# Kernel optimization log

Measured on AMD Instinct MI355X. Metric: run time of the kernel, lower is better.

The kernel has to match this reference:

```python
import jax, jax.numpy as jnp
import numpy as np

B, T_TEXT, HID = 16, 512, 512
MAX_LEN = 2048
DP_CH, DP_K = 256, 3
PP_CH, PP_K, PP_LAYERS = 384, 5, 5
N_BINS = 256


def conv1d_same(x, w, b, pad):
    # x: [B, C_in, T], w: [C_out, C_in, K] -> [B, C_out, T]
    xp = jnp.pad(x, ((0, 0), (0, 0), (pad, pad)))
    y = jax.lax.conv_general_dilated(xp, w, (1,), 'VALID',
                                     dimension_numbers=('NCH', 'OIH', 'NCH'))
    return y + b[None, :, None]


def channel_ln(x, g, beta, eps=1e-5):
    # LayerNorm over channel dim of [B, C, T] (torch LayerNorm with dim=1)
    m = jnp.mean(x, axis=1, keepdims=True)
    v = jnp.mean((x - m) ** 2, axis=1, keepdims=True)
    return (x - m) / jnp.sqrt(v + eps) * g[None, :, None] + beta[None, :, None]


def sinusoidal_pos(T, dim):
    # fairseq-style sinusoidal embedding, positions start at padding_idx+1 = 1
    half = dim // 2
    inv = jnp.exp(jnp.arange(half, dtype=jnp.float32) * (-np.log(10000.0) / (half - 1)))
    pos = jnp.arange(1, T + 1, dtype=jnp.float32)
    ang = pos[:, None] * inv[None, :]
    return jnp.concatenate([jnp.sin(ang), jnp.cos(ang)], axis=1)  # [T, dim]


def setup_inputs() -> dict:
    key = jax.random.key(0)
    ks = jax.random.split(key, 16)
    sd = lambda fan: 1.0 / np.sqrt(fan)
    inp = {}
    inp['x'] = jax.random.normal(ks[0], (B, T_TEXT, HID), dtype=jnp.float32)
    inp['duration'] = jax.random.randint(ks[1], (B, T_TEXT), 0, 7, dtype=jnp.int32)
    inp['src_mask'] = jnp.zeros((B, T_TEXT), dtype=bool)
    inp['max_len'] = MAX_LEN
    # duration predictor params (2 conv layers + linear)
    inp['dp_w0'] = jax.random.normal(ks[2], (DP_CH, HID, DP_K)) * sd(HID * DP_K)
    inp['dp_w1'] = jax.random.normal(ks[3], (DP_CH, DP_CH, DP_K)) * sd(DP_CH * DP_K)
    inp['dp_b'] = jnp.zeros((2, DP_CH))
    inp['dp_g'] = jnp.ones((2, DP_CH))
    inp['dp_beta'] = jnp.zeros((2, DP_CH))
    inp['dp_lin_w'] = jax.random.normal(ks[4], (DP_CH, 1)) * sd(DP_CH)
    inp['dp_lin_b'] = jnp.zeros((1,))
    # pitch predictor params (5 conv layers + linear, odim=2 for use_uv)
    inp['pp_w0'] = jax.random.normal(ks[5], (PP_CH, HID, PP_K)) * sd(HID * PP_K)
    inp['pp_w_rest'] = jax.random.normal(ks[6], (PP_LAYERS - 1, PP_CH, PP_CH, PP_K)) * sd(PP_CH * PP_K)
    inp['pp_b'] = jnp.zeros((PP_LAYERS, PP_CH))
    inp['pp_g'] = jnp.ones((PP_LAYERS, PP_CH))
    inp['pp_beta'] = jnp.zeros((PP_LAYERS, PP_CH))
    inp['pp_lin_w'] = jax.random.normal(ks[7], (PP_CH, 2)) * sd(PP_CH)
    inp['pp_lin_b'] = jnp.zeros((2,))
    inp['pos_alpha'] = jnp.ones((1,))
    inp['pitch_emb'] = jax.random.normal(ks[8], (N_BINS, HID)) * 0.02
    inp['pitch_bins'] = jnp.linspace(-1.0, 1.0, N_BINS - 1)  # linear quantization, stats min/max
    return inp


def reference(x, duration, src_mask, max_len, dp_w0, dp_w1, dp_b, dp_g, dp_beta,
              dp_lin_w, dp_lin_b, pp_w0, pp_w_rest, pp_b, pp_g, pp_beta,
              pp_lin_w, pp_lin_b, pos_alpha, pitch_emb, pitch_bins):
    Bn, T, H = x.shape
    keep = 1.0 - src_mask.astype(x.dtype)  # [B,T], 1 where valid

    # ---- DurationPredictor (log-domain durations) ----
    h = jnp.transpose(x, (0, 2, 1))  # [B,H,T]
    for i, w in enumerate([dp_w0, dp_w1]):
        h = conv1d_same(h, w, dp_b[i], (DP_K - 1) // 2)
        h = jax.nn.relu(h)
        h = channel_ln(h, dp_g[i], dp_beta[i])
        h = h * keep[:, None, :]
    log_dur = (jnp.einsum('bct,co->bto', h, dp_lin_w) + dp_lin_b) * keep[:, :, None]
    log_dur = log_dur[..., 0]  # [B,T]

    # ---- LengthRegulator: vectorized variable-repeat via searchsorted ----
    cum = jnp.cumsum(duration, axis=1)  # [B,T]
    frames = jnp.arange(max_len)
    tok = jax.vmap(lambda c: jnp.searchsorted(c, frames, side='right'))(cum)  # [B,max_len]
    mel_len = cum[:, -1]
    fmask = (frames[None, :] < mel_len[:, None]).astype(x.dtype)  # [B,max_len]
    mel = jnp.take_along_axis(x, jnp.minimum(tok, T - 1)[..., None], axis=1) * fmask[..., None]

    # ---- VariancePredictor (pitch, odim=2 for f0 + uv) ----
    pe = sinusoidal_pos(max_len, H)  # [max_len, H]
    p = mel + pos_alpha[0] * pe[None]
    p = jnp.transpose(p, (0, 2, 1))  # [B,H,max_len]
    for i in range(PP_LAYERS):
        w = pp_w0 if i == 0 else pp_w_rest[i - 1]
        p = conv1d_same(p, w, pp_b[i], (PP_K - 1) // 2)
        p = jax.nn.relu(p)
        p = channel_ln(p, pp_g[i], pp_beta[i])
    pitch_pred = jnp.einsum('bct,co->bto', p, pp_lin_w) + pp_lin_b  # [B,max_len,2]

    # ---- bucketize f0 channel + embedding add ----
    idx = jnp.searchsorted(pitch_bins, pitch_pred[..., 0], side='left')  # torch.bucketize
    p_embed = pitch_emb[idx]  # [B,max_len,H]
    out = mel + p_embed
    return out, log_dur, pitch_pred, mel_len
```

## Files before the change

kernel.cpp:

```cpp
#include <hip/hip_runtime.h>
#include <cstdint>
#include <cstddef>

constexpr int BB      = 16;
constexpr int T_TEXT  = 512;
constexpr int HID     = 512;
constexpr int MAX_LEN = 2048;
constexpr int DP_CH   = 256;
constexpr int PP_CH   = 384;

typedef unsigned short u16;
typedef unsigned int   u32;
typedef short bf16x8 __attribute__((ext_vector_type(8)));
typedef float f32x4  __attribute__((ext_vector_type(4)));

__device__ __forceinline__ void gload_lds16(const void* g, void* l) {
  __builtin_amdgcn_global_load_lds(
      (const __attribute__((address_space(1))) u32*)g,
      (__attribute__((address_space(3))) u32*)l, 16, 0, 0);
}

template <int N> __device__ __forceinline__ void vm_wait() {
  if constexpr (N == 0)      asm volatile("s_waitcnt vmcnt(0)" ::: "memory");
  else if constexpr (N == 3) asm volatile("s_waitcnt vmcnt(3)" ::: "memory");
  else if constexpr (N == 5) asm volatile("s_waitcnt vmcnt(5)" ::: "memory");
  else static_assert(N == 0, "unsupported vmcnt literal");
}

__device__ __forceinline__ u16 f2bf(float v) {
  union { float f; u32 u; } a;
  a.f = v;
  u32 r = (a.u + 0x7FFFu + ((a.u >> 16) & 1u)) >> 16;
  return (u16)r;
}
__device__ __forceinline__ float bf2f(u16 h) {
  union { u32 u; float f; } a;
  a.u = (u32)h << 16;
  return a.f;
}

__global__ __launch_bounds__(256) void pack_w_k(const float* __restrict__ w,
                                                u16* __restrict__ p,
                                                int O, int I, int KT) {
  int NF  = O >> 4, NCB = I >> 5;
  int total = KT * NCB * NF * 64;
  int idx = blockIdx.x * 256 + threadIdx.x;
  if (idx >= total) return;
  int l  = idx & 63;
  int f  = (idx >> 6) % NF;
  int cb = ((idx >> 6) / NF) % NCB;
  int k  = (idx >> 6) / (NF * NCB);
  int o  = f * 16 + (l & 15);
  int ib = cb * 32 + (l >> 4) * 8;
  u16* pd = p + ((size_t)((k * NCB + cb) * NF + f)) * 512 + (size_t)l * 8;
#pragma unroll
  for (int j = 0; j < 8; ++j)
    pd[j] = f2bf(w[((size_t)o * I + ib + j) * KT + k]);
}

template <int CIN, int COUT, int KT, int MT, int WM, int WN, int OPAD,
          bool F32OUT, bool COUNTED>
__global__ __launch_bounds__(WM * WN * 64)
void gemm_conv_ln(const u16* __restrict__ a, const u16* __restrict__ wp,
                  const float* __restrict__ bias, const float* __restrict__ gamma,
                  const float* __restrict__ beta,
                  u16* __restrict__ o, float* __restrict__ fo, int T) {
  constexpr int WAVES   = WM * WN;
  constexpr int THREADS = WAVES * 64;
  constexpr int RS    = MT + KT - 1;
  constexpr int NCB   = CIN / 32;
  constexpr int NF    = COUT / 16;
  constexpr int Mfr   = MT / (16 * WM);
  constexpr int Nfr   = NF / WN;
  constexpr int A_ONE = RS * 64;
  constexpr int B_ONE = NF * 1024;
  constexpr int B_OFF = 2 * A_ONE;
  constexpr int RED_OFF = B_OFF + 2 * B_ONE;
  static_assert(MT % (16 * WM) == 0 && NF % WN == 0, "tiling");
  static_assert((4 * RS) % WAVES == 0, "A chunks split evenly per wave");
  static_assert((NF * 64) % THREADS == 0, "B chunks split evenly");

  constexpr int CPW     = 4 * RS / WAVES;
  constexpr int A_INSTS = (CPW + 63) / 64;
  constexpr int VMB     = (NF * 64) / THREADS;
  constexpr int VMBA    = VMB + A_INSTS;

  const int TpIn  = T + KT - 1;
  const int TpOut = T + 2 * OPAD;

  const int tid  = threadIdx.x;
  const int wave = tid >> 6;
  const int lane = tid & 63;
  const int sl   = lane & 15;
  const int q    = lane >> 4;
  const int wm   = wave / WN;
  const int wn   = wave % WN;
  const int waveM0 = wm * Mfr * 16;
  const int f0   = wn * Nfr;
  const int t0   = blockIdx.x * MT;
  const int b    = blockIdx.y;

  extern __shared__ __align__(16) char smem[];

  const u16* abase_g = a + ((size_t)b * TpIn + t0) * CIN;

  auto stageA = [&](int buf, int cb) {
    char* lbase = smem + buf * A_ONE;
#pragma unroll
    for (int j = 0; j < CPW; j += 64) {
      int c   = wave * CPW + j + lane;
      int qc  = c / RS;
      int row = c - qc * RS;
      if (j + lane < CPW)
        gload_lds16(abase_g + (size_t)row * CIN + cb * 32 + qc * 8,
                    lbase + (size_t)(wave * CPW + j) * 16);
    }
  };
  auto stageB = [&](int buf, int k, int cb) {
    const u16* src = wp + ((size_t)(k * NCB + cb) * NF) * 512;
    char* lbase = smem + B_OFF + buf * B_ONE;
#pragma unroll
    for (int i = tid; i < NF * 64; i += THREADS) {
      gload_lds16(src + (size_t)i * 8, lbase + (size_t)(i - lane) * 16);
    }
  };

  f32x4 acc[Mfr][Nfr];
#pragma unroll
  for (int mf = 0; mf < Mfr; ++mf)
#pragma unroll
    for (int nf = 0; nf < Nfr; ++nf) acc[mf][nf] = (f32x4)0.f;

  stageA(0, 0);
  stageB(0, 0, 0);
  if constexpr (!COUNTED) {
    asm volatile("s_waitcnt vmcnt(0)" ::: "memory");
    __syncthreads();
  }

  int ab = 0, bb = 0;
  for (int cb = 0; cb < NCB; ++cb) {
    for (int k = 0; k < KT; ++k) {
      if (k + 1 < KT) {
        stageB(bb ^ 1, k + 1, cb);
        if constexpr (COUNTED) vm_wait<VMB>();
      } else if (cb + 1 < NCB) {
        stageB(bb ^ 1, 0, cb + 1);
        stageA(ab ^ 1, cb + 1);
        if constexpr (COUNTED) vm_wait<VMBA>();
      } else {
        if constexpr (COUNTED) vm_wait<0>();
      }
      if constexpr (COUNTED) {
        __builtin_amdgcn_s_barrier();
        __builtin_amdgcn_sched_barrier(0);
      }

      bf16x8 A[Mfr], Bf[Nfr];
      const char* ab_l = smem + ab * A_ONE;
#pragma unroll
      for (int mf = 0; mf < Mfr; ++mf) {
        int row = waveM0 + mf * 16 + sl + k;
        A[mf] = *(const bf16x8*)(ab_l + (q * RS + row) * 16);
      }
      const char* bb_l = smem + B_OFF + bb * B_ONE;
#pragma unroll
      for (int nf = 0; nf < Nfr; ++nf)
        Bf[nf] = *(const bf16x8*)(bb_l + (size_t)(f0 + nf) * 1024 + lane * 16);
#pragma unroll
      for (int nf = 0; nf < Nfr; ++nf)
#pragma unroll
        for (int mf = 0; mf < Mfr; ++mf)
          acc[mf][nf] = __builtin_amdgcn_mfma_f32_16x16x32_bf16(
              A[mf], Bf[nf], acc[mf][nf], 0, 0, 0);

      if constexpr (COUNTED) {
        __builtin_amdgcn_sched_barrier(0);
        __builtin_amdgcn_s_barrier();
      } else {
        asm volatile("s_waitcnt vmcnt(0)" ::: "memory");
        __syncthreads();
      }
      bb ^= 1;
      if (k == KT - 1) ab ^= 1;
    }
  }

  float bc[Nfr], gc[Nfr], btc[Nfr];
#pragma unroll
  for (int nf = 0; nf < Nfr; ++nf) {
    int col = (f0 + nf) * 16 + sl;
    bc[nf]  = bias[col];
    gc[nf]  = gamma[col];
    btc[nf] = beta[col];
  }

  float* reds  = (float*)(smem + RED_OFF);
  float* redss = reds + MT * WN;

#pragma unroll
  for (int mf = 0; mf < Mfr; ++mf) {
#pragma unroll
    for (int r = 0; r < 4; ++r) {
      float s = 0.f, ss2 = 0.f;
#pragma unroll
      for (int nf = 0; nf < Nfr; ++nf) {
        float x = acc[mf][nf][r] + bc[nf];
        x = fmaxf(x, 0.f);
        acc[mf][nf][r] = x;
        s += x;
        ss2 = fmaf(x, x, ss2);
      }
#pragma unroll
      for (int off = 1; off < 16; off <<= 1) {
        s   += __shfl_xor(s, off, 64);
        ss2 += __shfl_xor(ss2, off, 64);
      }
      if (sl == 0) {
        int rowb = waveM0 + mf * 16 + q * 4 + r;
        reds[rowb * WN + wn]  = s;
        redss[rowb * WN + wn] = ss2;
      }
    }
  }
  __syncthreads();

#pragma unroll
  for (int mf = 0; mf < Mfr; ++mf) {
#pragma unroll
    for (int r = 0; r < 4; ++r) {
      int rowb = waveM0 + mf * 16 + q * 4 + r;
      float s = 0.f, ss2 = 0.f;
#pragma unroll
      for (int w2 = 0; w2 < WN; ++w2) {
        s   += reds[rowb * WN + w2];
        ss2 += redss[rowb * WN + w2];
      }
      float mean = s * (1.f / COUT);
      float var  = ss2 * (1.f / COUT) - mean * mean;
      float rstd = 1.f / sqrtf(var + 1e-5f);
      int trow = t0 + rowb;
#pragma unroll
      for (int nf = 0; nf < Nfr; ++nf) {
        int col = (f0 + nf) * 16 + sl;
        float y = (acc[mf][nf][r] - mean) * rstd * gc[nf] + btc[nf];
        if constexpr (F32OUT) {
          fo[((size_t)b * T + trow) * COUT + col] = y;
        } else {
          o[((size_t)b * TpOut + OPAD + trow) * COUT + col] = f2bf(y);
        }
      }
    }
  }

  if constexpr (!F32OUT && OPAD > 0) {
    if (blockIdx.x == 0) {
      for (int i = tid; i < OPAD * COUT; i += THREADS) {
        o[(size_t)b * TpOut * COUT + i] = 0;
        o[((size_t)b * TpOut + OPAD + T) * COUT + i] = 0;
      }
    }
  }
}

constexpr int gemm_lds(int MT, int KT, int COUT, int WN_) {
  return 2 * (MT + KT - 1) * 64 + 2 * (COUT / 16) * 1024 + MT * WN_ * 8;
}

__global__ __launch_bounds__(256) void split_x_k(const float* __restrict__ x,
                                                 u16* __restrict__ xb) {
  int b = blockIdx.y;
  int row = blockIdx.x * 4 + (threadIdx.x >> 6);
  int lane = threadIdx.x & 63;
  if (row >= T_TEXT + 2) return;
  size_t out = ((size_t)b * (T_TEXT + 2) + row) * HID;
  if (row == 0 || row == T_TEXT + 1) {
    for (int h = lane; h < HID; h += 64) xb[out + h] = 0;
    return;
  }
  const float* xr = x + ((size_t)b * T_TEXT + row - 1) * HID;
  for (int h = lane; h < HID; h += 64) xb[out + h] = f2bf(xr[h]);
}

__global__ __launch_bounds__(256) void dp_head_k(const float* __restrict__ h,
                                                 const float* __restrict__ w,
                                                 const float* __restrict__ b,
                                                 float* __restrict__ out) {
  int tid = threadIdx.x;
  int wv = tid >> 6, lane = tid & 63;
  int row = blockIdx.x * 4 + wv;
  const float* hr = h + (size_t)row * DP_CH;
  float s = 0.f;
  for (int c = lane; c < DP_CH; c += 64) s = fmaf(hr[c], w[c], s);
#pragma unroll
  for (int off = 1; off < 64; off <<= 1) s += __shfl_xor(s, off, 64);
  if (lane == 0) out[row] = s + b[0];
}

__global__ __launch_bounds__(512) void cumsum_k(const int* __restrict__ dur,
                                                int* __restrict__ cum,
                                                float* __restrict__ mel_len_out) {
  __shared__ int s[T_TEXT];
  int b = blockIdx.x, t = threadIdx.x;
  s[t] = dur[b * T_TEXT + t];
  __syncthreads();
  for (int off = 1; off < T_TEXT; off <<= 1) {
    int add = (t >= off) ? s[t - off] : 0;
    __syncthreads();
    s[t] += add;
    __syncthreads();
  }
  cum[b * T_TEXT + t] = s[t];
  if (t == T_TEXT - 1) mel_len_out[b] = (float)s[t];
}

__global__ __launch_bounds__(256) void build_p_k(const float* __restrict__ x,
                                                 const int* __restrict__ cum,
                                                 const float* __restrict__ alpha_p,
                                                 u16* __restrict__ pb) {
  __shared__ int cs[T_TEXT];
  int b = blockIdx.y, tid = threadIdx.x;
  for (int i = tid; i < T_TEXT; i += 256) cs[i] = cum[b * T_TEXT + i];
  __syncthreads();
  int row = blockIdx.x * 4 + (tid >> 6);
  int lane = tid & 63;
  if (row >= MAX_LEN + 4) return;
  size_t out = ((size_t)b * (MAX_LEN + 4) + row) * HID;
  if (row < 2 || row >= MAX_LEN + 2) {
    for (int h = lane; h < HID; h += 64) pb[out + h] = 0;
    return;
  }
  int f = row - 2;
  int lo = 0, hi = T_TEXT;
  while (lo < hi) {
    int mid = (lo + hi) >> 1;
    if (cs[mid] <= f) lo = mid + 1; else hi = mid;
  }
  int src = min(lo, T_TEXT - 1);
  float fm = (f < cs[T_TEXT - 1]) ? 1.f : 0.f;
  float alpha = alpha_p[0];
  const float* xr = x + ((size_t)b * T_TEXT + src) * HID;
  float posf = (float)(f + 1);
  const float kfac = -0.03611898185f;
  for (int h = lane; h < HID / 2; h += 64) {
    float inv = expf((float)h * kfac);
    float ang = posf * inv;
    float sv, cv;
    sincosf(ang, &sv, &cv);
    pb[out + h]           = f2bf(fmaf(alpha, sv, xr[h] * fm));
    pb[out + h + HID / 2] = f2bf(fmaf(alpha, cv, xr[h + HID / 2] * fm));
  }
}

__global__ __launch_bounds__(256) void final_head_k(
    const u16* __restrict__ p, const float* __restrict__ x,
    const int* __restrict__ cum, const float* __restrict__ lw,
    const float* __restrict__ lb, const float* __restrict__ bins,
    const float* __restrict__ emb, float* __restrict__ out0,
    float* __restrict__ pred) {
  __shared__ int cs[T_TEXT];
  int b = blockIdx.y, tid = threadIdx.x;
  for (int i = tid; i < T_TEXT; i += 256) cs[i] = cum[b * T_TEXT + i];
  __syncthreads();
  int wv = tid >> 6, lane = tid & 63;
  int f = blockIdx.x * 4 + wv;
  size_t row = (size_t)b * MAX_LEN + f;
  const u16* prr = p + row * PP_CH;
  float s0 = 0.f, s1 = 0.f;
  for (int c = lane; c < PP_CH; c += 64) {
    float v = bf2f(prr[c]);
    s0 = fmaf(v, lw[2 * c], s0);
    s1 = fmaf(v, lw[2 * c + 1], s1);
  }
#pragma unroll
  for (int off = 1; off < 64; off <<= 1) {
    s0 += __shfl_xor(s0, off, 64);
    s1 += __shfl_xor(s1, off, 64);
  }
  float p0 = s0 + lb[0];
  float p1 = s1 + lb[1];
  if (lane == 0) {
    pred[row * 2] = p0;
    pred[row * 2 + 1] = p1;
  }
  int lo = 0, hi = 255;
  while (lo < hi) {
    int mid = (lo + hi) >> 1;
    if (bins[mid] < p0) lo = mid + 1; else hi = mid;
  }
  int lo2 = 0, hi2 = T_TEXT;
  while (lo2 < hi2) {
    int mid = (lo2 + hi2) >> 1;
    if (cs[mid] <= f) lo2 = mid + 1; else hi2 = mid;
  }
  int src = min(lo2, T_TEXT - 1);
  float fm = (f < cs[T_TEXT - 1]) ? 1.f : 0.f;
  const float* xr = x + ((size_t)b * T_TEXT + src) * HID;
  const float* er = emb + (size_t)lo * HID;
  float* orow = out0 + row * HID;
  for (int h = lane; h < HID; h += 64) orow[h] = fmaf(xr[h], fm, er[h]);
}

extern "C" void kernel_launch(void* const* d_in, const int* in_sizes, int n_in,
                              void* d_out, int out_size, void* d_ws,
                              size_t ws_size, hipStream_t stream) {
  (void)in_sizes; (void)n_in; (void)out_size; (void)ws_size;

  const float* x          = (const float*)d_in[0];
  const int*   duration   = (const int*)d_in[1];
  const float* dp_w0      = (const float*)d_in[4];
  const float* dp_w1      = (const float*)d_in[5];
  const float* dp_b       = (const float*)d_in[6];
  const float* dp_g       = (const float*)d_in[7];
  const float* dp_beta    = (const float*)d_in[8];
  const float* dp_lin_w   = (const float*)d_in[9];
  const float* dp_lin_b   = (const float*)d_in[10];
  const float* pp_w0      = (const float*)d_in[11];
  const float* pp_w_rest  = (const float*)d_in[12];
  const float* pp_b       = (const float*)d_in[13];
  const float* pp_g       = (const float*)d_in[14];
  const float* pp_beta    = (const float*)d_in[15];
  const float* pp_lin_w   = (const float*)d_in[16];
  const float* pp_lin_b   = (const float*)d_in[17];
  const float* pos_alpha  = (const float*)d_in[18];
  const float* pitch_emb  = (const float*)d_in[19];
  const float* pitch_bins = (const float*)d_in[20];

  char* w8 = (char*)d_ws;
  size_t off = 0;
  auto alloc = [&](size_t bytes) {
    char* pp = w8 + off;
    off += (bytes + 255) & ~(size_t)255;
    return pp;
  };
  u16*   xb    = (u16*)alloc((size_t)BB * 514 * 512 * 2);
  u16*   dp1   = (u16*)alloc((size_t)BB * 514 * 256 * 2);
  float* dp2   = (float*)alloc((size_t)BB * 512 * 256 * 4);
  u16*   Pb    = (u16*)alloc((size_t)BB * 2052 * 512 * 2);
  u16*   ppA   = (u16*)alloc((size_t)BB * 2052 * 384 * 2);
  u16*   ppB   = (u16*)alloc((size_t)BB * 2052 * 384 * 2);
  u16*   pfin  = (u16*)alloc((size_t)BB * 2048 * 384 * 2);
  u16*   pwdp0 = (u16*)alloc((size_t)3 * 512 * 256 * 2);
  u16*   pwdp1 = (u16*)alloc((size_t)3 * 256 * 256 * 2);
  u16*   pwpp0 = (u16*)alloc((size_t)5 * 512 * 384 * 2);
  u16*   pwppr = (u16*)alloc((size_t)4 * 5 * 384 * 384 * 2);
  int*   cum   = (int*)alloc((size_t)BB * T_TEXT * 4);

  float* out0       = (float*)d_out;
  float* log_dur    = out0 + (size_t)BB * MAX_LEN * HID;
  float* pitch_pred = log_dur + (size_t)BB * T_TEXT;
  float* mel_len    = pitch_pred + (size_t)BB * MAX_LEN * 2;

  auto pk = [&](const float* src, u16* dst, int O, int I, int KT) {
    int tot = KT * (I / 32) * (O / 16) * 64;
    pack_w_k<<<dim3((tot + 255) / 256), dim3(256), 0, stream>>>(src, dst, O, I, KT);
  };
  pk(dp_w0, pwdp0, 256, 512, 3);
  pk(dp_w1, pwdp1, 256, 256, 3);
  pk(pp_w0, pwpp0, 384, 512, 5);
  for (int l = 0; l < 4; ++l)
    pk(pp_w_rest + (size_t)l * 384 * 384 * 5,
       pwppr + (size_t)l * (5 * 384 * 384), 384, 384, 5);

  split_x_k<<<dim3(129, BB), dim3(256), 0, stream>>>(x, xb);
  cumsum_k<<<dim3(BB), dim3(512), 0, stream>>>(duration, cum, mel_len);

  constexpr int LDS_DP = gemm_lds(64, 3, 256, 2);
  gemm_conv_ln<512, 256, 3, 64, 2, 2, 1, false, false>
      <<<dim3(8, BB), dim3(256), LDS_DP, stream>>>(
          xb, pwdp0, dp_b, dp_g, dp_beta, dp1, nullptr, T_TEXT);
  gemm_conv_ln<256, 256, 3, 64, 2, 2, 1, true, false>
      <<<dim3(8, BB), dim3(256), LDS_DP, stream>>>(
          dp1, pwdp1, dp_b + 256, dp_g + 256, dp_beta + 256,
          nullptr, dp2, T_TEXT);
  dp_head_k<<<dim3(BB * T_TEXT / 4), dim3(256), 0, stream>>>(dp2, dp_lin_w,
                                                             dp_lin_b, log_dur);

  build_p_k<<<dim3(513, BB), dim3(256), 0, stream>>>(x, cum, pos_alpha, Pb);

  constexpr int LDS_PP = gemm_lds(128, 5, 384, 4);
  gemm_conv_ln<512, 384, 5, 128, 2, 4, 2, false, true>
      <<<dim3(16, BB), dim3(512), LDS_PP, stream>>>(
          Pb, pwpp0, pp_b, pp_g, pp_beta, ppA, nullptr, MAX_LEN);
  gemm_conv_ln<384, 384, 5, 128, 2, 4, 2, false, true>
      <<<dim3(16, BB), dim3(512), LDS_PP, stream>>>(
          ppA, pwppr + 0 * (5 * 384 * 384),
          pp_b + 384, pp_g + 384, pp_beta + 384, ppB, nullptr, MAX_LEN);
  gemm_conv_ln<384, 384, 5, 128, 2, 4, 2, false, true>
      <<<dim3(16, BB), dim3(512), LDS_PP, stream>>>(
          ppB, pwppr + 1 * (5 * 384 * 384),
          pp_b + 768, pp_g + 768, pp_beta + 768, ppA, nullptr, MAX_LEN);
  gemm_conv_ln<384, 384, 5, 128, 2, 4, 2, false, true>
      <<<dim3(16, BB), dim3(512), LDS_PP, stream>>>(
          ppA, pwppr + 2 * (5 * 384 * 384),
          pp_b + 1152, pp_g + 1152, pp_beta + 1152, ppB, nullptr, MAX_LEN);
  gemm_conv_ln<384, 384, 5, 128, 2, 4, 0, false, true>
      <<<dim3(16, BB), dim3(512), LDS_PP, stream>>>(
          ppB, pwppr + 3 * (5 * 384 * 384),
          pp_b + 1536, pp_g + 1536, pp_beta + 1536, pfin, nullptr, MAX_LEN);

  final_head_k<<<dim3(MAX_LEN / 4, BB), dim3(256), 0, stream>>>(
      pfin, x, cum, pp_lin_w, pp_lin_b, pitch_bins, pitch_emb, out0, pitch_pred);
}
```

Baseline: 421.3 us.

## Quad-buffer weight tiles and process two conv taps per barrier phase

In the counted path of the conv-GEMM+LayerNorm kernel, the weight (B) tiles move from double to quad buffering. The loop now prefetches two k-steps ahead and runs two MFMA steps between each pair of barriers, which halves barrier synchronisations and gives global-to-LDS loads more time to land. s_setprio is raised around the MFMA bursts to favour math issue. The cost is double the LDS used for B tiles, which can lower the number of blocks resident per CU. It also needs new vmcnt literals and an even total step count.

New measurement: 446.1 us. 5.9% more time.

```diff
diff --git a/kernel.cpp b/kernel.cpp
--- a/kernel.cpp
+++ b/kernel.cpp
@@ -22,8 +22,10 @@
 
 template <int N> __device__ __forceinline__ void vm_wait() {
   if constexpr (N == 0)      asm volatile("s_waitcnt vmcnt(0)" ::: "memory");
-  else if constexpr (N == 3) asm volatile("s_waitcnt vmcnt(3)" ::: "memory");
-  else if constexpr (N == 5) asm volatile("s_waitcnt vmcnt(5)" ::: "memory");
+  else if constexpr (N == 6) asm volatile("s_waitcnt vmcnt(6)" ::: "memory");
+  else if constexpr (N == 8) asm volatile("s_waitcnt vmcnt(8)" ::: "memory");
+  else if constexpr (N == 10) asm volatile("s_waitcnt vmcnt(10)" ::: "memory");
+  else if constexpr (N == 12) asm volatile("s_waitcnt vmcnt(12)" ::: "memory");
   else static_assert(N == 0, "unsupported vmcnt literal");
 }
 
@@ -75,7 +77,9 @@
   constexpr int A_ONE = RS * 64;
   constexpr int B_ONE = NF * 1024;
   constexpr int B_OFF = 2 * A_ONE;
-  constexpr int RED_OFF = B_OFF + 2 * B_ONE;
+  constexpr int NBUFB = 4;
+  constexpr int RED_OFF = B_OFF + NBUFB * B_ONE;
+  constexpr int NSTEPS = NCB * KT;
   static_assert(MT % (16 * WM) == 0 && NF % WN == 0, "tiling");
   static_assert((4 * RS) % WAVES == 0, "A chunks split evenly per wave");
   static_assert((NF * 64) % THREADS == 0, "B chunks split evenly");
@@ -83,7 +87,8 @@
   constexpr int CPW     = 4 * RS / WAVES;
   constexpr int A_INSTS = (CPW + 63) / 64;
   constexpr int VMB     = (NF * 64) / THREADS;
-  constexpr int VMBA    = VMB + A_INSTS;
+  constexpr int VM2B    = 2 * VMB;
+  constexpr int VM2BA   = 2 * VMB + A_INSTS;
 
   const int TpIn  = T + KT - 1;
   const int TpOut = T + 2 * OPAD;
@@ -131,58 +136,97 @@
 #pragma unroll
     for (int nf = 0; nf < Nfr; ++nf) acc[mf][nf] = (f32x4)0.f;
 
-  stageA(0, 0);
-  stageB(0, 0, 0);
-  if constexpr (!COUNTED) {
+  if constexpr (COUNTED) {
+    static_assert(NSTEPS % 2 == 0, "two-step phases need even step count");
+    stageA(0, 0);
+    stageB(0, 0, 0);
+    stageB(1, 1 % KT, 1 / KT);
+
+    for (int p = 0; p < NSTEPS / 2; ++p) {
+      const int s2 = 2 * p + 2;
+      if (s2 < NSTEPS) {
+        stageB(s2 & 3, s2 % KT, s2 / KT);
+        const int s3 = s2 + 1;
+        stageB(s3 & 3, s3 % KT, s3 / KT);
+        const int r = s2 % KT;
+        if (r == 0) {
+          stageA((s2 / KT) & 1, s2 / KT);
+          vm_wait<VM2BA>();
+        } else if (r == KT - 1) {
+          stageA((s3 / KT) & 1, s3 / KT);
+          vm_wait<VM2BA>();
+        } else {
+          vm_wait<VM2B>();
+        }
+      } else {
+        vm_wait<0>();
+      }
+      __builtin_amdgcn_s_barrier();
+      __builtin_amdgcn_sched_barrier(0);
+
+#pragma unroll
+      for (int u = 0; u < 2; ++u) {
+        const int s = 2 * p + u;
+        const int k = s % KT;
+        const char* ab_l = smem + ((s / KT) & 1) * A_ONE;
+        const char* bb_l = smem + B_OFF + (s & 3) * B_ONE;
+        bf16x8 A[Mfr], Bf[Nfr];
+#pragma unroll
+        for (int mf = 0; mf < Mfr; ++mf) {
+          int row = waveM0 + mf * 16 + sl + k;
+          A[mf] = *(const bf16x8*)(ab_l + (q * RS + row) * 16);
+        }
+#pragma unroll
+        for (int nf = 0; nf < Nfr; ++nf)
+          Bf[nf] = *(const bf16x8*)(bb_l + (size_t)(f0 + nf) * 1024 + lane * 16);
+        __builtin_amdgcn_s_setprio(1);
+#pragma unroll
+        for (int nf = 0; nf < Nfr; ++nf)
+#pragma unroll
+          for (int mf = 0; mf < Mfr; ++mf)
+            acc[mf][nf] = __builtin_amdgcn_mfma_f32_16x16x32_bf16(
+                A[mf], Bf[nf], acc[mf][nf], 0, 0, 0);
+        __builtin_amdgcn_s_setprio(0);
+      }
+      __builtin_amdgcn_sched_barrier(0);
+      __builtin_amdgcn_s_barrier();
+    }
+  } else {
+    stageA(0, 0);
+    stageB(0, 0, 0);
     asm volatile("s_waitcnt vmcnt(0)" ::: "memory");
     __syncthreads();
-  }
-
-  int ab = 0, bb = 0;
-  for (int cb = 0; cb < NCB; ++cb) {
-    for (int k = 0; k < KT; ++k) {
-      if (k + 1 < KT) {
-        stageB(bb ^ 1, k + 1, cb);
-        if constexpr (COUNTED) vm_wait<VMB>();
-      } else if (cb + 1 < NCB) {
-        stageB(bb ^ 1, 0, cb + 1);
-        stageA(ab ^ 1, cb + 1);
-        if constexpr (COUNTED) vm_wait<VMBA>();
-      } else {
-        if constexpr (COUNTED) vm_wait<0>();
-      }
-      if constexpr (COUNTED) {
-        __builtin_amdgcn_s_barrier();
-        __builtin_amdgcn_sched_barrier(0);
-      }
-
-      bf16x8 A[Mfr], Bf[Nfr];
-      const char* ab_l = smem + ab * A_ONE;
-#pragma unroll
-      for (int mf = 0; mf < Mfr; ++mf) {
-        int row = waveM0 + mf * 16 + sl + k;
-        A[mf] = *(const bf16x8*)(ab_l + (q * RS + row) * 16);
-      }
-      const char* bb_l = smem + B_OFF + bb * B_ONE;
-#pragma unroll
-      for (int nf = 0; nf < Nfr; ++nf)
-        Bf[nf] = *(const bf16x8*)(bb_l + (size_t)(f0 + nf) * 1024 + lane * 16);
-#pragma unroll
-      for (int nf = 0; nf < Nfr; ++nf)
-#pragma unroll
-        for (int mf = 0; mf < Mfr; ++mf)
-          acc[mf][nf] = __builtin_amdgcn_mfma_f32_16x16x32_bf16(
-              A[mf], Bf[nf], acc[mf][nf], 0, 0, 0);
-
-      if constexpr (COUNTED) {
-        __builtin_amdgcn_sched_barrier(0);
-        __builtin_amdgcn_s_barrier();
-      } else {
+    int ab = 0, bb = 0;
+    for (int cb = 0; cb < NCB; ++cb) {
+      for (int k = 0; k < KT; ++k) {
+        if (k + 1 < KT) {
+          stageB(bb ^ 1, k + 1, cb);
+        } else if (cb + 1 < NCB) {
+          stageB(bb ^ 1, 0, cb + 1);
+          stageA(ab ^ 1, cb + 1);
+        }
+        bf16x8 A[Mfr], Bf[Nfr];
+        const char* ab_l = smem + ab * A_ONE;
+#pragma unroll
+        for (int mf = 0; mf < Mfr; ++mf) {
+          int row = waveM0 + mf * 16 + sl + k;
+          A[mf] = *(const bf16x8*)(ab_l + (q * RS + row) * 16);
+        }
+        const char* bb_l = smem + B_OFF + bb * B_ONE;
+#pragma unroll
+        for (int nf = 0; nf < Nfr; ++nf)
+          Bf[nf] = *(const bf16x8*)(bb_l + (size_t)(f0 + nf) * 1024 + lane * 16);
+#pragma unroll
+        for (int nf = 0; nf < Nfr; ++nf)
+#pragma unroll
+          for (int mf = 0; mf < Mfr; ++mf)
+            acc[mf][nf] = __builtin_amdgcn_mfma_f32_16x16x32_bf16(
+                A[mf], Bf[nf], acc[mf][nf], 0, 0, 0);
         asm volatile("s_waitcnt vmcnt(0)" ::: "memory");
         __syncthreads();
-      }
-      bb ^= 1;
-      if (k == KT - 1) ab ^= 1;
+        bb ^= 1;
+        if (k == KT - 1) ab ^= 1;
+      }
     }
   }
 
@@ -264,7 +308,7 @@
 }
 
 constexpr int gemm_lds(int MT, int KT, int COUT, int WN_) {
-  return 2 * (MT + KT - 1) * 64 + 2 * (COUT / 16) * 1024 + MT * WN_ * 8;
+  return 2 * (MT + KT - 1) * 64 + 4 * (COUT / 16) * 1024 + MT * WN_ * 8;
 }
 
 __global__ __launch_bounds__(256) void split_x_k(const float* __restrict__ x,
```

## Stage all conv taps per channel block with per-wave tap rotation

Applied to the files above, without the earlier changes.

For the pitch-predictor convolutions, all KT weight taps for a channel block are loaded into LDS at once, replacing the per-tap double buffer. Each wave starts at a different tap to spread LDS bank traffic, and MFMA issue is raised with setprio. This cuts the barrier count from two per tap to two per channel block. In exchange, weight loads are no longer overlapped with compute, and the larger LDS footprint lowers occupancy. The non-rotating path drops its counted-wait option and always waits fully.

Result: slower. 443.1 us (+5.2%).

```diff
diff --git a/kernel.cpp b/kernel.cpp
--- a/kernel.cpp
+++ b/kernel.cpp
@@ -18,13 +18,6 @@
   __builtin_amdgcn_global_load_lds(
       (const __attribute__((address_space(1))) u32*)g,
       (__attribute__((address_space(3))) u32*)l, 16, 0, 0);
-}
-
-template <int N> __device__ __forceinline__ void vm_wait() {
-  if constexpr (N == 0)      asm volatile("s_waitcnt vmcnt(0)" ::: "memory");
-  else if constexpr (N == 3) asm volatile("s_waitcnt vmcnt(3)" ::: "memory");
-  else if constexpr (N == 5) asm volatile("s_waitcnt vmcnt(5)" ::: "memory");
-  else static_assert(N == 0, "unsupported vmcnt literal");
 }
 
 __device__ __forceinline__ u16 f2bf(float v) {
@@ -59,7 +52,7 @@
 }
 
 template <int CIN, int COUT, int KT, int MT, int WM, int WN, int OPAD,
-          bool F32OUT, bool COUNTED>
+          bool F32OUT, bool ROTATE>
 __global__ __launch_bounds__(WM * WN * 64)
 void gemm_conv_ln(const u16* __restrict__ a, const u16* __restrict__ wp,
                   const float* __restrict__ bias, const float* __restrict__ gamma,
@@ -75,15 +68,12 @@
   constexpr int A_ONE = RS * 64;
   constexpr int B_ONE = NF * 1024;
   constexpr int B_OFF = 2 * A_ONE;
-  constexpr int RED_OFF = B_OFF + 2 * B_ONE;
+  constexpr int NBUFB = ROTATE ? KT : 2;
+  constexpr int RED_OFF = B_OFF + NBUFB * B_ONE;
   static_assert(MT % (16 * WM) == 0 && NF % WN == 0, "tiling");
   static_assert((4 * RS) % WAVES == 0, "A chunks split evenly per wave");
   static_assert((NF * 64) % THREADS == 0, "B chunks split evenly");
-
-  constexpr int CPW     = 4 * RS / WAVES;
-  constexpr int A_INSTS = (CPW + 63) / 64;
-  constexpr int VMB     = (NF * 64) / THREADS;
-  constexpr int VMBA    = VMB + A_INSTS;
+  constexpr int CPW = 4 * RS / WAVES;
 
   const int TpIn  = T + KT - 1;
   const int TpOut = T + 2 * OPAD;
@@ -131,58 +121,84 @@
 #pragma unroll
     for (int nf = 0; nf < Nfr; ++nf) acc[mf][nf] = (f32x4)0.f;
 
-  stageA(0, 0);
-  stageB(0, 0, 0);
-  if constexpr (!COUNTED) {
+  if constexpr (ROTATE) {
+    stageA(0, 0);
+#pragma unroll
+    for (int j = 0; j < KT; ++j) stageB(j, j, 0);
     asm volatile("s_waitcnt vmcnt(0)" ::: "memory");
     __syncthreads();
-  }
-
-  int ab = 0, bb = 0;
-  for (int cb = 0; cb < NCB; ++cb) {
-    for (int k = 0; k < KT; ++k) {
-      if (k + 1 < KT) {
-        stageB(bb ^ 1, k + 1, cb);
-        if constexpr (COUNTED) vm_wait<VMB>();
-      } else if (cb + 1 < NCB) {
-        stageB(bb ^ 1, 0, cb + 1);
-        stageA(ab ^ 1, cb + 1);
-        if constexpr (COUNTED) vm_wait<VMBA>();
-      } else {
-        if constexpr (COUNTED) vm_wait<0>();
-      }
-      if constexpr (COUNTED) {
-        __builtin_amdgcn_s_barrier();
-        __builtin_amdgcn_sched_barrier(0);
-      }
-
-      bf16x8 A[Mfr], Bf[Nfr];
-      const char* ab_l = smem + ab * A_ONE;
-#pragma unroll
-      for (int mf = 0; mf < Mfr; ++mf) {
-        int row = waveM0 + mf * 16 + sl + k;
-        A[mf] = *(const bf16x8*)(ab_l + (q * RS + row) * 16);
-      }
-      const char* bb_l = smem + B_OFF + bb * B_ONE;
-#pragma unroll
-      for (int nf = 0; nf < Nfr; ++nf)
-        Bf[nf] = *(const bf16x8*)(bb_l + (size_t)(f0 + nf) * 1024 + lane * 16);
-#pragma unroll
-      for (int nf = 0; nf < Nfr; ++nf)
-#pragma unroll
-        for (int mf = 0; mf < Mfr; ++mf)
-          acc[mf][nf] = __builtin_amdgcn_mfma_f32_16x16x32_bf16(
-              A[mf], Bf[nf], acc[mf][nf], 0, 0, 0);
-
-      if constexpr (COUNTED) {
-        __builtin_amdgcn_sched_barrier(0);
-        __builtin_amdgcn_s_barrier();
-      } else {
+
+    const int r0 = wave % KT;
+    for (int cb = 0; cb < NCB; ++cb) {
+      if (cb + 1 < NCB) stageA((cb + 1) & 1, cb + 1);
+      const char* ab_l = smem + (cb & 1) * A_ONE;
+#pragma unroll
+      for (int t = 0; t < KT; ++t) {
+        int k = r0 + t;
+        if (k >= KT) k -= KT;
+        const char* bb_l = smem + B_OFF + k * B_ONE;
+        bf16x8 A[Mfr], Bf[Nfr];
+#pragma unroll
+        for (int mf = 0; mf < Mfr; ++mf) {
+          int row = waveM0 + mf * 16 + sl + k;
+          A[mf] = *(const bf16x8*)(ab_l + (q * RS + row) * 16);
+        }
+#pragma unroll
+        for (int nf = 0; nf < Nfr; ++nf)
+          Bf[nf] = *(const bf16x8*)(bb_l + (size_t)(f0 + nf) * 1024 + lane * 16);
+        __builtin_amdgcn_s_setprio(1);
+#pragma unroll
+        for (int nf = 0; nf < Nfr; ++nf)
+#pragma unroll
+          for (int mf = 0; mf < Mfr; ++mf)
+            acc[mf][nf] = __builtin_amdgcn_mfma_f32_16x16x32_bf16(
+                A[mf], Bf[nf], acc[mf][nf], 0, 0, 0);
+        __builtin_amdgcn_s_setprio(0);
+      }
+      __syncthreads();
+      if (cb + 1 < NCB) {
+#pragma unroll
+        for (int j = 0; j < KT; ++j) stageB(j, j, cb + 1);
         asm volatile("s_waitcnt vmcnt(0)" ::: "memory");
         __syncthreads();
       }
-      bb ^= 1;
-      if (k == KT - 1) ab ^= 1;
+    }
+  } else {
+    stageA(0, 0);
+    stageB(0, 0, 0);
+    asm volatile("s_waitcnt vmcnt(0)" ::: "memory");
+    __syncthreads();
+    int ab = 0, bb = 0;
+    for (int cb = 0; cb < NCB; ++cb) {
+      for (int k = 0; k < KT; ++k) {
+        if (k + 1 < KT) {
+          stageB(bb ^ 1, k + 1, cb);
+        } else if (cb + 1 < NCB) {
+          stageB(bb ^ 1, 0, cb + 1);
+          stageA(ab ^ 1, cb + 1);
+        }
+        bf16x8 A[Mfr], Bf[Nfr];
+        const char* ab_l = smem + ab * A_ONE;
+#pragma unroll
+        for (int mf = 0; mf < Mfr; ++mf) {
+          int row = waveM0 + mf * 16 + sl + k;
+          A[mf] = *(const bf16x8*)(ab_l + (q * RS + row) * 16);
+        }
+        const char* bb_l = smem + B_OFF + bb * B_ONE;
+#pragma unroll
+        for (int nf = 0; nf < Nfr; ++nf)
+          Bf[nf] = *(const bf16x8*)(bb_l + (size_t)(f0 + nf) * 1024 + lane * 16);
+#pragma unroll
+        for (int nf = 0; nf < Nfr; ++nf)
+#pragma unroll
+          for (int mf = 0; mf < Mfr; ++mf)
+            acc[mf][nf] = __builtin_amdgcn_mfma_f32_16x16x32_bf16(
+                A[mf], Bf[nf], acc[mf][nf], 0, 0, 0);
+        asm volatile("s_waitcnt vmcnt(0)" ::: "memory");
+        __syncthreads();
+        bb ^= 1;
+        if (k == KT - 1) ab ^= 1;
+      }
     }
   }
 
@@ -263,8 +279,8 @@
   }
 }
 
-constexpr int gemm_lds(int MT, int KT, int COUT, int WN_) {
-  return 2 * (MT + KT - 1) * 64 + 2 * (COUT / 16) * 1024 + MT * WN_ * 8;
+constexpr int gemm_lds(int MT, int KT, int COUT, int WN_, int nbufb) {
+  return 2 * (MT + KT - 1) * 64 + nbufb * (COUT / 16) * 1024 + MT * WN_ * 8;
 }
 
 __global__ __launch_bounds__(256) void split_x_k(const float* __restrict__ x,
@@ -465,7 +481,7 @@
   split_x_k<<<dim3(129, BB), dim3(256), 0, stream>>>(x, xb);
   cumsum_k<<<dim3(BB), dim3(512), 0, stream>>>(duration, cum, mel_len);
 
-  constexpr int LDS_DP = gemm_lds(64, 3, 256, 2);
+  constexpr int LDS_DP = gemm_lds(64, 3, 256, 2, 2);
   gemm_conv_ln<512, 256, 3, 64, 2, 2, 1, false, false>
       <<<dim3(8, BB), dim3(256), LDS_DP, stream>>>(
           xb, pwdp0, dp_b, dp_g, dp_beta, dp1, nullptr, T_TEXT);
@@ -478,7 +494,7 @@
 
   build_p_k<<<dim3(513, BB), dim3(256), 0, stream>>>(x, cum, pos_alpha, Pb);
 
-  constexpr int LDS_PP = gemm_lds(128, 5, 384, 4);
+  constexpr int LDS_PP = gemm_lds(128, 5, 384, 4, 5);
   gemm_conv_ln<512, 384, 5, 128, 2, 4, 2, false, true>
       <<<dim3(16, BB), dim3(512), LDS_PP, stream>>>(
           Pb, pwpp0, pp_b, pp_g, pp_beta, ppA, nullptr, MAX_LEN);
```
